# Optimization experiments

Measured on AMD Instinct MI355X. Metric: run time of the kernel, lower is better.

Reference implementation:

```python
import jax, jax.numpy as jnp
import numpy as np

B, S, H, L, NH, DH, FF = 64, 256, 768, 12, 12, 64, 3072
V, MAXP, NTYPE, NI, NS = 30522, 512, 2, 10, 64


def setup_inputs() -> dict:
    key = jax.random.key(0)
    ks = iter(jax.random.split(key, 40))
    n = lambda shp, s=0.02: jax.random.normal(next(ks), shp, jnp.float32) * s
    inp = {
        'input_ids': jax.random.randint(next(ks), (B, S), 0, V),
        'attention_mask': jnp.ones((B, S), jnp.int32),
        'token_type_ids': jnp.zeros((B, S), jnp.int32),
        'intent_labels': jax.random.randint(next(ks), (B,), 0, NI),
        'slot_labels': jax.random.randint(next(ks), (B, S), 0, NS),
        'word_emb': n((V, H)), 'pos_emb': n((MAXP, H)), 'type_emb': n((NTYPE, H)),
        'emb_ln_g': jnp.ones((H,)), 'emb_ln_b': jnp.zeros((H,)),
        'Wq': n((L, H, H)), 'bq': jnp.zeros((L, H)),
        'Wk': n((L, H, H)), 'bk': jnp.zeros((L, H)),
        'Wv': n((L, H, H)), 'bv': jnp.zeros((L, H)),
        'Wo': n((L, H, H)), 'bo': jnp.zeros((L, H)),
        'ln1_g': jnp.ones((L, H)), 'ln1_b': jnp.zeros((L, H)),
        'W1': n((L, H, FF)), 'b1': jnp.zeros((L, FF)),
        'W2': n((L, FF, H)), 'b2': jnp.zeros((L, H)),
        'ln2_g': jnp.ones((L, H)), 'ln2_b': jnp.zeros((L, H)),
        'Wi': n((H, NI)), 'bi': jnp.zeros((NI,)),
        'Ws': n((H, NS)), 'bs': jnp.zeros((NS,)),
        'crf_start': n((NS,), 0.1), 'crf_end': n((NS,), 0.1),
        'crf_trans': n((NS, NS), 0.1),
    }
    return inp


def _ln(x, g, b):
    m = x.mean(-1, keepdims=True)
    v = jnp.square(x - m).mean(-1, keepdims=True)
    return (x - m) * jax.lax.rsqrt(v + 1e-12) * g + b


def _forward(params, input_ids, attention_mask, token_type_ids, intent_labels, slot_labels):
    (word_emb, pos_emb, type_emb, emb_ln_g, emb_ln_b,
     Wq, bq, Wk, bk, Wv, bv, Wo, bo, ln1_g, ln1_b,
     W1, b1, W2, b2, ln2_g, ln2_b,
     Wi, bi, Ws, bs, crf_start, crf_end, crf_trans) = params
    Bn, Sn = input_ids.shape
    Hn = word_emb.shape[1]
    dh = Hn // NH
    # BERT embeddings (dropout is identity in eval)
    x = word_emb[input_ids] + pos_emb[:Sn][None] + type_emb[token_type_ids]
    x = _ln(x, emb_ln_g, emb_ln_b)
    bias = (1.0 - attention_mask.astype(x.dtype))[:, None, None, :] * -1e9  # [B,1,1,S]

    def layer(h, p):
        wq, cq, wk, ck, wv, cv, wo, co, g1, d1, w1, e1, w2, e2, g2, d2 = p
        q = (h @ wq + cq).reshape(Bn, Sn, NH, dh)
        k = (h @ wk + ck).reshape(Bn, Sn, NH, dh)
        v = (h @ wv + cv).reshape(Bn, Sn, NH, dh)
        sc = jnp.einsum('bqnd,bknd->bnqk', q, k) / jnp.sqrt(jnp.float32(dh)) + bias
        a = jax.nn.softmax(sc, axis=-1)
        ctx = jnp.einsum('bnqk,bknd->bqnd', a, v).reshape(Bn, Sn, Hn)
        h2 = _ln(h + ctx @ wo + co, g1, d1)
        ff = jax.nn.gelu(h2 @ w1 + e1, approximate=False)
        return _ln(h2 + ff @ w2 + e2, g2, d2), None

    x, _ = jax.lax.scan(layer, x, (Wq, bq, Wk, bk, Wv, bv, Wo, bo,
                                   ln1_g, ln1_b, W1, b1, W2, b2, ln2_g, ln2_b))
    intent_logits = x[:, 0, :] @ Wi + bi           # [B, NI]
    slot_logits = x @ Ws + bs                      # [B, S, NS]
    # intent cross-entropy (mean over batch)
    lp = jax.nn.log_softmax(intent_logits, axis=-1)
    intent_loss = -jnp.take_along_axis(lp, intent_labels[:, None], axis=1).mean()
    # CRF log-likelihood
    mask = attention_mask.astype(slot_logits.dtype)
    em, tags = slot_logits, slot_labels
    t0 = tags[:, 0]
    score = crf_start[t0] + jnp.take_along_axis(em[:, 0, :], t0[:, None], axis=1)[:, 0]
    prev, cur = tags[:, :-1], tags[:, 1:]
    step_sc = crf_trans[prev, cur] + jnp.take_along_axis(em[:, 1:, :], cur[..., None], axis=2)[..., 0]
    score = score + (step_sc * mask[:, 1:]).sum(1)
    lengths = attention_mask.sum(1)
    last_tag = jnp.take_along_axis(tags, (lengths - 1)[:, None].astype(tags.dtype), axis=1)[:, 0]
    score = score + crf_end[last_tag]
    em_t = jnp.swapaxes(em, 0, 1)    # [S,B,C]
    mk_t = jnp.swapaxes(mask, 0, 1)  # [S,B]
    alpha0 = crf_start[None, :] + em_t[0]

    def crf_step(alpha, xs):
        e, m = xs
        nxt = jax.scipy.special.logsumexp(alpha[:, :, None] + crf_trans[None], axis=1) + e
        return jnp.where(m[:, None] > 0, nxt, alpha), None

    alpha, _ = jax.lax.scan(crf_step, alpha0, (em_t[1:], mk_t[1:]))
    logZ = jax.scipy.special.logsumexp(alpha + crf_end[None, :], axis=1)
    llh = score - logZ                # per-sequence log-likelihood
    crf_loss = -llh.mean()
    return intent_loss + 2.0 * crf_loss


def reference(input_ids, attention_mask, token_type_ids, intent_labels, slot_labels,
              word_emb, pos_emb, type_emb, emb_ln_g, emb_ln_b,
              Wq, bq, Wk, bk, Wv, bv, Wo, bo, ln1_g, ln1_b,
              W1, b1, W2, b2, ln2_g, ln2_b,
              Wi, bi, Ws, bs, crf_start, crf_end, crf_trans):
    params = (word_emb, pos_emb, type_emb, emb_ln_g, emb_ln_b,
              Wq, bq, Wk, bk, Wv, bv, Wo, bo, ln1_g, ln1_b,
              W1, b1, W2, b2, ln2_g, ln2_b,
              Wi, bi, Ws, bs, crf_start, crf_end, crf_trans)
    return _forward(params, input_ids, attention_mask, token_type_ids, intent_labels, slot_labels)
```

## Files before the change

kernel.cpp:

```cpp
#include <hip/hip_runtime.h>
#include <stdint.h>

typedef unsigned short u16;
typedef __attribute__((ext_vector_type(8))) short bh8;
typedef __attribute__((ext_vector_type(4))) float f4;

#define DEV static __device__ __forceinline__

DEV u16 f2bf(float f){ union{float f; uint32_t u;} v; v.f=f; uint32_t r=v.u + 0x7FFFu + ((v.u>>16)&1u); return (u16)(r>>16); }
DEV float bf2f(u16 u){ union{uint32_t u; float f;} v; v.u=((uint32_t)u)<<16; return v.f; }

DEV void mfma16(f4& d, bh8 a, bh8 b){
  asm("v_mfma_f32_16x16x32_bf16 %0, %1, %2, %0" : "+v"(d) : "v"(a), "v"(b));
}

#define FENCE16(A) asm volatile("s_nop 7\ns_nop 7" : \
 "+v"(A[0][0]),"+v"(A[0][1]),"+v"(A[0][2]),"+v"(A[0][3]),\
 "+v"(A[1][0]),"+v"(A[1][1]),"+v"(A[1][2]),"+v"(A[1][3]),\
 "+v"(A[2][0]),"+v"(A[2][1]),"+v"(A[2][2]),"+v"(A[2][3]),\
 "+v"(A[3][0]),"+v"(A[3][1]),"+v"(A[3][2]),"+v"(A[3][3]))

#define GLD16(g,l) __builtin_amdgcn_global_load_lds( \
    (__attribute__((address_space(1))) void*)(void*)(g), \
    (__attribute__((address_space(3))) void*)(void*)(l), 16, 0, 0)

struct GemmP { const u16* A; const u16* B; int K; void* C; int ldc;
               const float* b0; const float* b1; const float* b2; const u16* res; };

template<int EPI>
__global__ __launch_bounds__(256)
void gemm_bt(GemmP p){
  __shared__ __align__(16) u16 As[128*32];
  __shared__ __align__(16) u16 Bs[128*32];
  const int t=threadIdx.x, l=t&63, w=t>>6, wr=w>>1, wc=w&1;
  const int m0=blockIdx.x*128, n0=blockIdx.y*128;
  const u16* Ab = p.A + (size_t)m0*p.K;
  const u16* Bb = p.B + (size_t)n0*p.K;
  const int srow=l>>2, scol=(l&3)*8;
  f4 acc[4][4] = {};
  for(int k0=0;k0<p.K;k0+=32){
#pragma unroll
    for(int i=0;i<2;i++){
      const int c=w*2+i;
      GLD16(Ab + (size_t)(c*16+srow)*p.K + k0 + scol, &As[c*512]);
      GLD16(Bb + (size_t)(c*16+srow)*p.K + k0 + scol, &Bs[c*512]);
    }
    __syncthreads();
    bh8 af[4], bfr[4];
#pragma unroll
    for(int m=0;m<4;m++) af[m] = *(const bh8*)&As[(wr*64+m*16+(l&15))*32 + (l>>4)*8];
#pragma unroll
    for(int n=0;n<4;n++) bfr[n] = *(const bh8*)&Bs[(wc*64+n*16+(l&15))*32 + (l>>4)*8];
#pragma unroll
    for(int m=0;m<4;m++)
#pragma unroll
      for(int n=0;n<4;n++) mfma16(acc[m][n], af[m], bfr[n]);
    __syncthreads();
  }
  FENCE16(acc);
  const int lc=l&15, lr=(l>>4)*4;
#pragma unroll
  for(int m=0;m<4;m++)
#pragma unroll
  for(int n=0;n<4;n++)
#pragma unroll
  for(int r=0;r<4;r++){
    const int gr = m0 + wr*64 + m*16 + lr + r;
    const int gc = n0 + wc*64 + n*16 + lc;
    float v = acc[m][n][r];
    if(EPI==0){
      const float* bp = (gc<768)? p.b0 : (gc<1536? p.b1 : p.b2);
      const int bc = (gc<768)? gc : (gc<1536? gc-768 : gc-1536);
      ((u16*)p.C)[(size_t)gr*p.ldc + gc] = f2bf(v + bp[bc]);
    } else if(EPI==1){
      v += p.b0[gc] + bf2f(p.res[(size_t)gr*p.ldc + gc]);
      ((u16*)p.C)[(size_t)gr*p.ldc + gc] = f2bf(v);
    } else if(EPI==2){
      v += p.b0[gc];
      v = 0.5f*v*(1.f + erff(v*0.70710678118f));
      ((u16*)p.C)[(size_t)gr*p.ldc + gc] = f2bf(v);
    } else {
      v += (gc<64)? p.b0[gc] : 0.f;
      ((float*)p.C)[(size_t)gr*p.ldc + gc] = v;
    }
  }
}

__global__ __launch_bounds__(256)
void attn_kernel(const u16* __restrict__ qkv, const int* __restrict__ amask, u16* __restrict__ ctx){
  __shared__ __align__(16) u16 Ks[256*64];
  __shared__ __align__(16) u16 Vt[64*256];
  __shared__ __align__(16) u16 Ps[4*64*64];
  __shared__ float biasS[256];
  const int t=threadIdx.x, l=t&63, w=t>>6;
  const int b=blockIdx.x/12, h=blockIdx.x%12;
  biasS[t] = (1.f - (float)amask[b*256+t]) * -1e9f;
  const u16* kb = qkv + ((size_t)b*256)*2304 + 768 + h*64;
  const u16* vb = kb + 768;
#pragma unroll
  for(int i=0;i<8;i++){
    const int c = t + i*256;
    const int row = c>>3, seg = c&7;
    uint4 kv = *(const uint4*)(kb + (size_t)row*2304 + seg*8);
    const int ba = row*128 + seg*16;
    *(uint4*)((char*)Ks + (ba ^ ((row&7)<<4))) = kv;
    uint4 vv = *(const uint4*)(vb + (size_t)row*2304 + seg*8);
    const u16* pv = (const u16*)&vv;
#pragma unroll
    for(int j=0;j<8;j++){
      const int d = seg*8+j;
      const int bb = d*512 + row*2;
      *(u16*)((char*)Vt + (bb ^ ((d&7)<<4))) = pv[j];
    }
  }
  bh8 aq[4][2];
  const u16* qb = qkv + ((size_t)b*256 + w*64)*2304 + h*64;
#pragma unroll
  for(int m=0;m<4;m++)
#pragma unroll
    for(int ks=0;ks<2;ks++)
      aq[m][ks] = *(const bh8*)(qb + (size_t)(m*16+(l&15))*2304 + ks*32 + (l>>4)*8);
  __syncthreads();
  float mrun[4][4], lrun[4][4];
  f4 o[4][4] = {};
#pragma unroll
  for(int m=0;m<4;m++)
#pragma unroll
    for(int r=0;r<4;r++){ mrun[m][r] = -3e38f; lrun[m][r]=0.f; }
  u16* Pw = Ps + w*4096;
  for(int kt=0;kt<4;kt++){
    f4 sacc[4][4] = {};
#pragma unroll
    for(int ks=0;ks<2;ks++)
#pragma unroll
      for(int n=0;n<4;n++){
        const int row = kt*64 + n*16 + (l&15);
        const int by = row*128 + ks*64 + (l>>4)*16;
        bh8 bk = *(const bh8*)((const char*)Ks + (by ^ ((row&7)<<4)));
#pragma unroll
        for(int m=0;m<4;m++) mfma16(sacc[m][n], aq[m][ks], bk);
      }
    FENCE16(sacc);
#pragma unroll
    for(int m=0;m<4;m++){
      float rmax[4] = {-3e38f,-3e38f,-3e38f,-3e38f};
#pragma unroll
      for(int n=0;n<4;n++){
        const float bi = biasS[kt*64 + n*16 + (l&15)];
#pragma unroll
        for(int r=0;r<4;r++){
          float sv = sacc[m][n][r]*0.125f + bi;
          sacc[m][n][r] = sv;
          rmax[r] = fmaxf(rmax[r], sv);
        }
      }
#pragma unroll
      for(int dd=1; dd<16; dd<<=1)
#pragma unroll
        for(int r=0;r<4;r++) rmax[r] = fmaxf(rmax[r], __shfl_xor(rmax[r], dd));
      float psum[4];
#pragma unroll
      for(int r=0;r<4;r++){
        const float mn = fmaxf(mrun[m][r], rmax[r]);
        const float corr = __expf(mrun[m][r] - mn);
        mrun[m][r] = mn;
        lrun[m][r] *= corr;
#pragma unroll
        for(int nd=0; nd<4; nd++) o[m][nd][r] *= corr;
        psum[r] = 0.f;
      }
#pragma unroll
      for(int n=0;n<4;n++)
#pragma unroll
        for(int r=0;r<4;r++){
          const float pvv = __expf(sacc[m][n][r] - mrun[m][r]);
          sacc[m][n][r] = pvv;
          psum[r] += pvv;
        }
#pragma unroll
      for(int dd=1; dd<16; dd<<=1)
#pragma unroll
        for(int r=0;r<4;r++) psum[r] += __shfl_xor(psum[r], dd);
#pragma unroll
      for(int r=0;r<4;r++) lrun[m][r] += psum[r];
#pragma unroll
      for(int n=0;n<4;n++)
#pragma unroll
        for(int r=0;r<4;r++){
          const int prow = m*16 + (l>>4)*4 + r;
          const int pcol = n*16 + (l&15);
          const int by = prow*128 + pcol*2;
          *(u16*)((char*)Pw + (by ^ ((prow&7)<<4))) = f2bf(sacc[m][n][r]);
        }
    }
#pragma unroll
    for(int ks=0;ks<2;ks++){
      bh8 ap[4];
#pragma unroll
      for(int m=0;m<4;m++){
        const int prow = m*16 + (l&15);
        const int by = prow*128 + (ks*32 + (l>>4)*8)*2;
        ap[m] = *(const bh8*)((const char*)Pw + (by ^ ((prow&7)<<4)));
      }
#pragma unroll
      for(int nd=0; nd<4; nd++){
        const int dR = nd*16 + (l&15);
        const int by = dR*512 + (kt*64 + ks*32 + (l>>4)*8)*2;
        bh8 bv = *(const bh8*)((const char*)Vt + (by ^ ((dR&7)<<4)));
#pragma unroll
        for(int m=0;m<4;m++) mfma16(o[m][nd], ap[m], bv);
      }
    }
  }
  FENCE16(o);
#pragma unroll
  for(int m=0;m<4;m++)
#pragma unroll
  for(int nd=0; nd<4; nd++)
#pragma unroll
  for(int r=0;r<4;r++){
    const int row = w*64 + m*16 + (l>>4)*4 + r;
    const float vv = o[m][nd][r] / lrun[m][r];
    ctx[((size_t)b*256 + row)*768 + h*64 + nd*16 + (l&15)] = f2bf(vv);
  }
}

__global__ void ln_kernel(const u16* __restrict__ in, const float* __restrict__ g,
                          const float* __restrict__ b, u16* __restrict__ out){
  const int row = blockIdx.x, t = threadIdx.x;
  __shared__ float red[8];
  const u16* rp = in + (size_t)row*768;
  float v[3]; float s=0.f, q=0.f;
#pragma unroll
  for(int i=0;i<3;i++){ float x = bf2f(rp[t + i*256]); v[i]=x; s+=x; q+=x*x; }
#pragma unroll
  for(int dd=1; dd<64; dd<<=1){ s += __shfl_xor(s,dd); q += __shfl_xor(q,dd); }
  if((t&63)==0){ red[t>>6]=s; red[4+(t>>6)]=q; }
  __syncthreads();
  s = red[0]+red[1]+red[2]+red[3];
  q = red[4]+red[5]+red[6]+red[7];
  const float mean = s*(1.f/768.f);
  float var = q*(1.f/768.f) - mean*mean; var = fmaxf(var, 0.f);
  const float rs = rsqrtf(var + 1e-12f);
  u16* op = out + (size_t)row*768;
#pragma unroll
  for(int i=0;i<3;i++){ const int hh=t+i*256; op[hh] = f2bf((v[i]-mean)*rs*g[hh] + b[hh]); }
}

__global__ void embed_ln(const int* __restrict__ ids, const int* __restrict__ tti,
    const float* __restrict__ we, const float* __restrict__ pe, const float* __restrict__ te,
    const float* __restrict__ g, const float* __restrict__ bb, u16* __restrict__ x){
  const int tok = blockIdx.x, t = threadIdx.x;
  __shared__ float red[8];
  const int id = ids[tok], tyid = tti[tok], s0 = tok & 255;
  float v[3]; float s=0.f,q=0.f;
#pragma unroll
  for(int i=0;i<3;i++){
    const int hh = t+i*256;
    float x0 = we[(size_t)id*768+hh] + pe[(size_t)s0*768+hh] + te[(size_t)tyid*768+hh];
    v[i]=x0; s+=x0; q+=x0*x0;
  }
#pragma unroll
  for(int dd=1; dd<64; dd<<=1){ s += __shfl_xor(s,dd); q += __shfl_xor(q,dd); }
  if((t&63)==0){ red[t>>6]=s; red[4+(t>>6)]=q; }
  __syncthreads();
  s = red[0]+red[1]+red[2]+red[3];
  q = red[4]+red[5]+red[6]+red[7];
  const float mean = s*(1.f/768.f);
  float var = q*(1.f/768.f) - mean*mean; var = fmaxf(var, 0.f);
  const float rs = rsqrtf(var + 1e-12f);
#pragma unroll
  for(int i=0;i<3;i++){ const int hh=t+i*256; x[(size_t)tok*768+hh] = f2bf((v[i]-mean)*rs*g[hh] + bb[hh]); }
}

__global__ void transpose_cvt(const float* __restrict__ src, u16* __restrict__ dst, int R, int C){
  __shared__ float sm[32][33];
  const int ntc = C>>5;
  const int tr = blockIdx.x/ntc, tc = blockIdx.x - tr*ntc;
  const int r0 = tr<<5, c0 = tc<<5;
  const int tx = threadIdx.x, ty2 = threadIdx.y;
#pragma unroll
  for(int i=0;i<4;i++) sm[ty2+i*8][tx] = src[(size_t)(r0+ty2+i*8)*C + c0+tx];
  __syncthreads();
#pragma unroll
  for(int i=0;i<4;i++) dst[(size_t)(c0+ty2+i*8)*R + r0+tx] = f2bf(sm[tx][ty2+i*8]);
}

__global__ void conv_layer(const float* __restrict__ Wq, const float* __restrict__ Wk,
    const float* __restrict__ Wv, const float* __restrict__ Wo,
    const float* __restrict__ W1, const float* __restrict__ W2, u16* __restrict__ Wt){
  __shared__ float sm[32][33];
  const int bid = blockIdx.x;
  const float* src; u16* dst; int R, C, tt;
  if(bid<2304){
    R=768; C=768; const int mi = bid/576; tt = bid - mi*576;
    src = (mi==0?Wq: mi==1?Wk: mi==2?Wv: Wo);
    dst = Wt + (size_t)mi*589824;
  } else if(bid<4608){ R=768; C=3072; tt=bid-2304; src=W1; dst=Wt+2359296; }
  else { R=3072; C=768; tt=bid-4608; src=W2; dst=Wt+4718592; }
  const int ntc=C>>5; const int tr=tt/ntc, tc=tt-tr*ntc;
  const int r0=tr<<5, c0=tc<<5, tx=threadIdx.x, ty2=threadIdx.y;
#pragma unroll
  for(int i=0;i<4;i++) sm[ty2+i*8][tx] = src[(size_t)(r0+ty2+i*8)*C + c0+tx];
  __syncthreads();
#pragma unroll
  for(int i=0;i<4;i++) dst[(size_t)(c0+ty2+i*8)*R + r0+tx] = f2bf(sm[tx][ty2+i*8]);
}

__global__ void intent_kernel(const u16* __restrict__ x, const float* __restrict__ Wi,
    const float* __restrict__ bi, const int* __restrict__ lab, float* __restrict__ parts){
  const int b = blockIdx.x, t = threadIdx.x;
  __shared__ float xs[768];
  __shared__ float lg[10];
  const u16* rp = x + ((size_t)b*256)*768;
#pragma unroll
  for(int i=0;i<3;i++) xs[t+i*256] = bf2f(rp[t+i*256]);
  __syncthreads();
  if(t<10){
    float s = bi[t];
    for(int k=0;k<768;k++) s += xs[k]*Wi[(size_t)k*10 + t];
    lg[t] = s;
  }
  __syncthreads();
  if(t==0){
    float m = lg[0];
    for(int j=1;j<10;j++) m = fmaxf(m, lg[j]);
    float se = 0.f;
    for(int j=0;j<10;j++) se += expf(lg[j]-m);
    parts[b] = (logf(se) + m) - lg[lab[b]];
  }
}

__global__ __launch_bounds__(64)
void crf_kernel(const float* __restrict__ em, const int* __restrict__ tags,
    const int* __restrict__ amask, const float* __restrict__ cs, const float* __restrict__ ce,
    const float* __restrict__ tr, float* __restrict__ parts){
  const int b = blockIdx.x, j = threadIdx.x;
  const float* eb = em + (size_t)b*256*128;
  const int* tg = tags + b*256;
  const int* mk = amask + b*256;
  __shared__ __align__(16) float aS[64];
  float Etr[64];
#pragma unroll
  for(int i=0;i<64;i++) Etr[i] = __expf(tr[i*64 + j]);
  float sc = 0.f; int len = 0;
  for(int s=j+1; s<256; s+=64){
    const int pv = tg[s-1], cu = tg[s];
    sc += (tr[pv*64+cu] + eb[(size_t)s*128+cu]) * (float)mk[s];
  }
  for(int s=j; s<256; s+=64) len += mk[s];
#pragma unroll
  for(int dd=1; dd<64; dd<<=1){ sc += __shfl_xor(sc,dd); len += __shfl_xor(len,dd); }
  const int t0 = tg[0];
  float score = sc + cs[t0] + eb[t0] + ce[tg[len-1]];
  float a = __expf(cs[j] + eb[j]);
  float logc = 0.f;
  float em_s = eb[128 + j];
  int   mk_s = mk[1];
  for(int s=1; s<256; s++){
    const int sn = (s<255)? s+1 : s;
    const float em_n = eb[(size_t)sn*128 + j];
    const int   mk_n = mk[sn];
    aS[j] = a;
    __syncthreads();
    float acc0=0.f, acc1=0.f, acc2=0.f, acc3=0.f;
    const float4* ap = (const float4*)aS;
#pragma unroll
    for(int q2=0;q2<16;q2++){
      const float4 av = ap[q2];
      acc0 += av.x*Etr[4*q2+0];
      acc1 += av.y*Etr[4*q2+1];
      acc2 += av.z*Etr[4*q2+2];
      acc3 += av.w*Etr[4*q2+3];
    }
    __syncthreads();
    const float nxt = ((acc0+acc1)+(acc2+acc3)) * __expf(em_s);
    a = (mk_s > 0) ? nxt : a;
    if((s&7)==7){
      const float c = __shfl(a, 0);
      logc += __logf(c);
      a *= (1.f/c);
    }
    em_s = em_n; mk_s = mk_n;
  }
  float v2 = logf(a) + logc + ce[j];
  float am2 = v2;
#pragma unroll
  for(int dd=1; dd<64; dd<<=1) am2 = fmaxf(am2, __shfl_xor(am2,dd));
  float se = __expf(v2 - am2);
#pragma unroll
  for(int dd=1; dd<64; dd<<=1) se += __shfl_xor(se,dd);
  if(j==0) parts[64+b] = (logf(se)+am2) - score;
}

__global__ void final_reduce(const float* __restrict__ parts, float* __restrict__ out){
  const int t = threadIdx.x;
  float a = parts[t], c = parts[64+t];
#pragma unroll
  for(int dd=1; dd<64; dd<<=1){ a += __shfl_xor(a,dd); c += __shfl_xor(c,dd); }
  if(t==0) out[0] = a*(1.f/64.f) + 2.f*c*(1.f/64.f);
}

extern "C" void kernel_launch(void* const* d_in, const int* in_sizes, int n_in,
                              void* d_out, int out_size, void* d_ws, size_t ws_size,
                              hipStream_t stream){
  (void)in_sizes; (void)n_in; (void)out_size;
  const int* ids   = (const int*)d_in[0];
  const int* amask = (const int*)d_in[1];
  const int* tti   = (const int*)d_in[2];
  const int* ilab  = (const int*)d_in[3];
  const int* slab  = (const int*)d_in[4];
  const float* we  = (const float*)d_in[5];
  const float* pe  = (const float*)d_in[6];
  const float* te  = (const float*)d_in[7];
  const float* eg  = (const float*)d_in[8];
  const float* ebt = (const float*)d_in[9];
  const float* Wq  = (const float*)d_in[10];
  const float* bq  = (const float*)d_in[11];
  const float* Wk  = (const float*)d_in[12];
  const float* bkk = (const float*)d_in[13];
  const float* Wv  = (const float*)d_in[14];
  const float* bvv = (const float*)d_in[15];
  const float* Wo  = (const float*)d_in[16];
  const float* bo  = (const float*)d_in[17];
  const float* l1g = (const float*)d_in[18];
  const float* l1b = (const float*)d_in[19];
  const float* W1  = (const float*)d_in[20];
  const float* b1  = (const float*)d_in[21];
  const float* W2  = (const float*)d_in[22];
  const float* b2  = (const float*)d_in[23];
  const float* l2g = (const float*)d_in[24];
  const float* l2b = (const float*)d_in[25];
  const float* Wi  = (const float*)d_in[26];
  const float* bi  = (const float*)d_in[27];
  const float* Wsp = (const float*)d_in[28];
  const float* bs  = (const float*)d_in[29];
  const float* cs  = (const float*)d_in[30];
  const float* ce  = (const float*)d_in[31];
  const float* ctr = (const float*)d_in[32];

  char* ws = (char*)d_ws;
  size_t off = 0;
  auto alloc = [&](size_t bytes)->void*{ void* p = ws + off; off += (bytes+255)&~(size_t)255; return p; };
  u16* x     = (u16*)alloc(16384ull*768*2);
  u16* h2    = (u16*)alloc(16384ull*768*2);
  u16* y     = (u16*)alloc(16384ull*768*2);
  u16* qkv   = (u16*)alloc(16384ull*2304*2);
  u16* cf    = (u16*)alloc(16384ull*3072*2);
  u16* Wt    = (u16*)alloc(7077888ull*2);
  u16* WsT   = (u16*)alloc(128ull*768*2);
  float* slots = (float*)alloc(16384ull*128*4);
  float* parts = (float*)alloc(512);
  if(off > ws_size) return;

  dim3 T256(256), T328(32,8);
  embed_ln<<<dim3(16384), T256, 0, stream>>>(ids, tti, we, pe, te, eg, ebt, x);
  transpose_cvt<<<dim3(48), T328, 0, stream>>>(Wsp, WsT, 768, 64);
  for(int L=0; L<12; L++){
    const size_t oH = (size_t)L*768*768, oF = (size_t)L*768*3072;
    conv_layer<<<dim3(6912), T328, 0, stream>>>(Wq+oH, Wk+oH, Wv+oH, Wo+oH, W1+oF, W2+oF, Wt);
    GemmP pq{ x, Wt, 768, qkv, 2304, bq+L*768, bkk+L*768, bvv+L*768, nullptr };
    gemm_bt<0><<<dim3(128,18), T256, 0, stream>>>(pq);
    attn_kernel<<<dim3(768), T256, 0, stream>>>(qkv, amask, cf);
    GemmP po{ cf, Wt+1769472, 768, y, 768, bo+L*768, nullptr, nullptr, x };
    gemm_bt<1><<<dim3(128,6), T256, 0, stream>>>(po);
    ln_kernel<<<dim3(16384), T256, 0, stream>>>(y, l1g+L*768, l1b+L*768, h2);
    GemmP p1{ h2, Wt+2359296, 768, cf, 3072, b1+L*3072, nullptr, nullptr, nullptr };
    gemm_bt<2><<<dim3(128,24), T256, 0, stream>>>(p1);
    GemmP p2{ cf, Wt+4718592, 3072, y, 768, b2+L*768, nullptr, nullptr, h2 };
    gemm_bt<1><<<dim3(128,6), T256, 0, stream>>>(p2);
    ln_kernel<<<dim3(16384), T256, 0, stream>>>(y, l2g+L*768, l2b+L*768, x);
  }
  GemmP psl{ x, WsT, 768, slots, 128, bs, nullptr, nullptr, nullptr };
  gemm_bt<3><<<dim3(128,1), T256, 0, stream>>>(psl);
  intent_kernel<<<dim3(64), T256, 0, stream>>>(x, Wi, bi, ilab, parts);
  crf_kernel<<<dim3(64), dim3(64), 0, stream>>>(slots, slab, amask, cs, ce, ctr, parts);
  final_reduce<<<dim3(1), dim3(64), 0, stream>>>(parts, (float*)d_out);
}
```

Before: 5.481 ms.

## Add pipelined 256x256 GEMM for QKV/FFN1 and widen K tiles to 64

Adds a 512-thread 256x256-tile GEMM with double-buffered LDS (128KB dynamic), XOR-swizzled layout, interleaved global-to-LDS prefetch and s_setprio around the MFMA groups, and uses it for the QKV and FFN1 projections. The existing 128x128 GEMM moves to a K-step of 64 with swizzled LDS. Inline-asm MFMA and the nop fences are replaced by the compiler builtin. GELU's erff is replaced by a polynomial erf approximation. Together these aim to raise MFMA utilisation and cut barrier and epilogue cost, at the risk of tail imbalance from fewer blocks and small accuracy loss in GELU.

```diff
diff --git a/kernel.cpp b/kernel.cpp
--- a/kernel.cpp
+++ b/kernel.cpp
@@ -11,14 +11,18 @@
 DEV float bf2f(u16 u){ union{uint32_t u; float f;} v; v.u=((uint32_t)u)<<16; return v.f; }
 
 DEV void mfma16(f4& d, bh8 a, bh8 b){
-  asm("v_mfma_f32_16x16x32_bf16 %0, %1, %2, %0" : "+v"(d) : "v"(a), "v"(b));
-}
-
-#define FENCE16(A) asm volatile("s_nop 7\ns_nop 7" : \
- "+v"(A[0][0]),"+v"(A[0][1]),"+v"(A[0][2]),"+v"(A[0][3]),\
- "+v"(A[1][0]),"+v"(A[1][1]),"+v"(A[1][2]),"+v"(A[1][3]),\
- "+v"(A[2][0]),"+v"(A[2][1]),"+v"(A[2][2]),"+v"(A[2][3]),\
- "+v"(A[3][0]),"+v"(A[3][1]),"+v"(A[3][2]),"+v"(A[3][3]))
+  d = __builtin_amdgcn_mfma_f32_16x16x32_bf16(a, b, d, 0, 0, 0);
+}
+
+DEV float gelu(float v){
+  float x = v*0.70710678118f;
+  float ax = fabsf(x);
+  float tt = 1.0f/(1.0f + 0.3275911f*ax);
+  float y = 1.0f - (((((1.061405429f*tt - 1.453152027f)*tt) + 1.421413741f)*tt
+                     - 0.284496736f)*tt + 0.254829592f)*tt*__expf(-ax*ax);
+  float e = (x<0.f)? -y : y;
+  return 0.5f*v*(1.0f+e);
+}
 
 #define GLD16(g,l) __builtin_amdgcn_global_load_lds( \
     (__attribute__((address_space(1))) void*)(void*)(g), \
@@ -28,61 +32,184 @@
                const float* b0; const float* b1; const float* b2; const u16* res; };
 
 template<int EPI>
+DEV void epi_store(const GemmP& p, int gr, int gc, float v){
+  if(EPI==0){
+    const float* bp = (gc<768)? p.b0 : (gc<1536? p.b1 : p.b2);
+    const int bc = (gc<768)? gc : (gc<1536? gc-768 : gc-1536);
+    ((u16*)p.C)[(size_t)gr*p.ldc + gc] = f2bf(v + bp[bc]);
+  } else if(EPI==1){
+    v += p.b0[gc] + bf2f(p.res[(size_t)gr*p.ldc + gc]);
+    ((u16*)p.C)[(size_t)gr*p.ldc + gc] = f2bf(v);
+  } else if(EPI==2){
+    ((u16*)p.C)[(size_t)gr*p.ldc + gc] = f2bf(gelu(v + p.b0[gc]));
+  } else {
+    v += (gc<64)? p.b0[gc] : 0.f;
+    ((float*)p.C)[(size_t)gr*p.ldc + gc] = v;
+  }
+}
+
+template<int EPI>
+__global__ __launch_bounds__(512)
+void gemm256(GemmP p){
+  extern __shared__ char smem[];
+  const int t=threadIdx.x, l=t&63, w=t>>6;
+  const int wr=w>>2, wc=w&3;
+  const int m0=blockIdx.x*256, n0=blockIdx.y*256;
+  const int K=p.K, NT=K>>6;
+  const int fl=l&15, fh=l>>4;
+
+  const int r0=(w*1024+l*16)>>7;
+  const int cs=(((l&7)^(l>>3))<<4);
+  const char* gA0 = (const char*)p.A + ((size_t)(m0+r0)*K)*2 + cs;
+  const char* gB0 = (const char*)p.B + ((size_t)(n0+r0)*K)*2 + cs;
+  const size_t rowblk = (size_t)64*K*2;
+  char* dA = smem + w*1024;
+  char* dB = smem + 32768 + w*1024;
+
+  #define SG_A(T,h,buf) do{ const char* _s=gA0 + (size_t)(T)*128 + (size_t)(h)*2*rowblk; \
+    char* _d=dA+(buf)*65536+(h)*16384; GLD16(_s,_d); GLD16(_s+rowblk,_d+8192); }while(0)
+  #define SG_B(T,h,buf) do{ const char* _s=gB0 + (size_t)(T)*128 + (size_t)(h)*2*rowblk; \
+    char* _d=dB+(buf)*65536+(h)*16384; GLD16(_s,_d); GLD16(_s+rowblk,_d+8192); }while(0)
+
+  int oB[4][2], oA[8][2];
+#pragma unroll
+  for(int nf=0;nf<4;nf++){ const int rw=wc*64+nf*16+fl;
+#pragma unroll
+    for(int ks=0;ks<2;ks++) oB[nf][ks] = 32768 + rw*128 + ((ks*64+fh*16) ^ ((rw&7)<<4)); }
+#pragma unroll
+  for(int mf=0;mf<8;mf++){ const int rw=wr*128+mf*16+fl;
+#pragma unroll
+    for(int ks=0;ks<2;ks++) oA[mf][ks] = rw*128 + ((ks*64+fh*16) ^ ((rw&7)<<4)); }
+
+  f4 acc[8][4] = {};
+  bh8 bf_[4][2], af_[2][2];
+
+  #define MFMA_Q(q) do{ \
+    __builtin_amdgcn_s_setprio(1); \
+    _Pragma("unroll") \
+    for(int j=0;j<2;j++) \
+      _Pragma("unroll") \
+      for(int nf=0;nf<4;nf++){ mfma16(acc[2*(q)+j][nf], af_[j][0], bf_[nf][0]); \
+                               mfma16(acc[2*(q)+j][nf], af_[j][1], bf_[nf][1]); } \
+    __builtin_amdgcn_s_setprio(0); }while(0)
+
+  #define WAIT_LGKM do{ asm volatile("s_waitcnt lgkmcnt(0)":::"memory"); \
+    __builtin_amdgcn_sched_barrier(0); }while(0)
+
+  SG_A(0,0,0); SG_A(0,1,0); SG_B(0,0,0); SG_B(0,1,0);
+  if(NT>1){ SG_B(1,0,1); SG_B(1,1,1);
+            asm volatile("s_waitcnt vmcnt(4)":::"memory"); }
+  else    { asm volatile("s_waitcnt vmcnt(0)":::"memory"); }
+  __builtin_amdgcn_s_barrier();
+
+  for(int T=0; T<NT; ++T){
+    const int cur=T&1, nxt=cur^1;
+    const char* sb = smem + (cur<<16);
+    if(T+1<NT){ SG_A(T+1,0,nxt); SG_A(T+1,1,nxt); }
+#pragma unroll
+    for(int nf=0;nf<4;nf++){ bf_[nf][0]=*(const bh8*)(sb+oB[nf][0]); bf_[nf][1]=*(const bh8*)(sb+oB[nf][1]); }
+    af_[0][0]=*(const bh8*)(sb+oA[0][0]); af_[0][1]=*(const bh8*)(sb+oA[0][1]);
+    af_[1][0]=*(const bh8*)(sb+oA[1][0]); af_[1][1]=*(const bh8*)(sb+oA[1][1]);
+    __builtin_amdgcn_s_barrier();
+    WAIT_LGKM;
+    MFMA_Q(0);
+    __builtin_amdgcn_s_barrier();
+    if(T+2<NT) SG_B(T+2,0,cur);
+    af_[0][0]=*(const bh8*)(sb+oA[2][0]); af_[0][1]=*(const bh8*)(sb+oA[2][1]);
+    af_[1][0]=*(const bh8*)(sb+oA[3][0]); af_[1][1]=*(const bh8*)(sb+oA[3][1]);
+    __builtin_amdgcn_s_barrier();
+    WAIT_LGKM;
+    MFMA_Q(1);
+    __builtin_amdgcn_s_barrier();
+    if(T+2<NT) SG_B(T+2,1,cur);
+    af_[0][0]=*(const bh8*)(sb+oA[4][0]); af_[0][1]=*(const bh8*)(sb+oA[4][1]);
+    af_[1][0]=*(const bh8*)(sb+oA[5][0]); af_[1][1]=*(const bh8*)(sb+oA[5][1]);
+    __builtin_amdgcn_s_barrier();
+    WAIT_LGKM;
+    MFMA_Q(2);
+    __builtin_amdgcn_s_barrier();
+    af_[0][0]=*(const bh8*)(sb+oA[6][0]); af_[0][1]=*(const bh8*)(sb+oA[6][1]);
+    af_[1][0]=*(const bh8*)(sb+oA[7][0]); af_[1][1]=*(const bh8*)(sb+oA[7][1]);
+    if(T+2<NT)      asm volatile("s_waitcnt vmcnt(4)":::"memory");
+    else if(T+1<NT) asm volatile("s_waitcnt vmcnt(0)":::"memory");
+    __builtin_amdgcn_s_barrier();
+    WAIT_LGKM;
+    MFMA_Q(3);
+    __builtin_amdgcn_s_barrier();
+  }
+  #undef SG_A
+  #undef SG_B
+  #undef MFMA_Q
+  #undef WAIT_LGKM
+
+  const int lr=fh*4;
+#pragma unroll
+  for(int m=0;m<8;m++)
+#pragma unroll
+  for(int n=0;n<4;n++)
+#pragma unroll
+  for(int r=0;r<4;r++){
+    epi_store<EPI>(p, m0 + wr*128 + m*16 + lr + r, n0 + wc*64 + n*16 + fl, acc[m][n][r]);
+  }
+}
+
+template<int EPI>
 __global__ __launch_bounds__(256)
 void gemm_bt(GemmP p){
-  __shared__ __align__(16) u16 As[128*32];
-  __shared__ __align__(16) u16 Bs[128*32];
+  __shared__ __align__(16) u16 As[128*64];
+  __shared__ __align__(16) u16 Bs[128*64];
   const int t=threadIdx.x, l=t&63, w=t>>6, wr=w>>1, wc=w&1;
+  const int fl=l&15, fh=l>>4;
   const int m0=blockIdx.x*128, n0=blockIdx.y*128;
-  const u16* Ab = p.A + (size_t)m0*p.K;
-  const u16* Bb = p.B + (size_t)n0*p.K;
-  const int srow=l>>2, scol=(l&3)*8;
+  const int K=p.K, NT=K>>6;
+  const int srow=t>>3;
+  const int cs=(((t&7) ^ (srow&7))<<4);
+  const char* gA = (const char*)p.A + ((size_t)(m0+srow)*K)*2 + cs;
+  const char* gB = (const char*)p.B + ((size_t)(n0+srow)*K)*2 + cs;
+  const size_t r32 = (size_t)32*K*2;
+  char* dA = (char*)As + t*16;
+  char* dB = (char*)Bs + t*16;
+
+  int oA2[4][2], oB2[4][2];
+#pragma unroll
+  for(int mf=0;mf<4;mf++){ const int rw=wr*64+mf*16+fl;
+#pragma unroll
+    for(int ks=0;ks<2;ks++) oA2[mf][ks] = rw*128 + ((ks*64+fh*16) ^ ((rw&7)<<4)); }
+#pragma unroll
+  for(int nf=0;nf<4;nf++){ const int rw=wc*64+nf*16+fl;
+#pragma unroll
+    for(int ks=0;ks<2;ks++) oB2[nf][ks] = rw*128 + ((ks*64+fh*16) ^ ((rw&7)<<4)); }
+
   f4 acc[4][4] = {};
-  for(int k0=0;k0<p.K;k0+=32){
-#pragma unroll
-    for(int i=0;i<2;i++){
-      const int c=w*2+i;
-      GLD16(Ab + (size_t)(c*16+srow)*p.K + k0 + scol, &As[c*512]);
-      GLD16(Bb + (size_t)(c*16+srow)*p.K + k0 + scol, &Bs[c*512]);
-    }
+  for(int T=0; T<NT; ++T){
+#pragma unroll
+    for(int j=0;j<4;j++) GLD16(gA + (size_t)T*128 + j*r32, dA + j*4096);
+#pragma unroll
+    for(int j=0;j<4;j++) GLD16(gB + (size_t)T*128 + j*r32, dB + j*4096);
     __syncthreads();
-    bh8 af[4], bfr[4];
-#pragma unroll
-    for(int m=0;m<4;m++) af[m] = *(const bh8*)&As[(wr*64+m*16+(l&15))*32 + (l>>4)*8];
-#pragma unroll
-    for(int n=0;n<4;n++) bfr[n] = *(const bh8*)&Bs[(wc*64+n*16+(l&15))*32 + (l>>4)*8];
-#pragma unroll
-    for(int m=0;m<4;m++)
-#pragma unroll
-      for(int n=0;n<4;n++) mfma16(acc[m][n], af[m], bfr[n]);
+    bh8 af[4][2], bfr[4][2];
+#pragma unroll
+    for(int mf=0;mf<4;mf++){ af[mf][0]=*(const bh8*)((const char*)As+oA2[mf][0]);
+                             af[mf][1]=*(const bh8*)((const char*)As+oA2[mf][1]); }
+#pragma unroll
+    for(int nf=0;nf<4;nf++){ bfr[nf][0]=*(const bh8*)((const char*)Bs+oB2[nf][0]);
+                             bfr[nf][1]=*(const bh8*)((const char*)Bs+oB2[nf][1]); }
+#pragma unroll
+    for(int ks=0;ks<2;ks++)
+#pragma unroll
+      for(int m=0;m<4;m++)
+#pragma unroll
+        for(int n=0;n<4;n++) mfma16(acc[m][n], af[m][ks], bfr[n][ks]);
     __syncthreads();
   }
-  FENCE16(acc);
-  const int lc=l&15, lr=(l>>4)*4;
+  const int lr=fh*4;
 #pragma unroll
   for(int m=0;m<4;m++)
 #pragma unroll
   for(int n=0;n<4;n++)
 #pragma unroll
   for(int r=0;r<4;r++){
-    const int gr = m0 + wr*64 + m*16 + lr + r;
-    const int gc = n0 + wc*64 + n*16 + lc;
-    float v = acc[m][n][r];
-    if(EPI==0){
-      const float* bp = (gc<768)? p.b0 : (gc<1536? p.b1 : p.b2);
-      const int bc = (gc<768)? gc : (gc<1536? gc-768 : gc-1536);
-      ((u16*)p.C)[(size_t)gr*p.ldc + gc] = f2bf(v + bp[bc]);
-    } else if(EPI==1){
-      v += p.b0[gc] + bf2f(p.res[(size_t)gr*p.ldc + gc]);
-      ((u16*)p.C)[(size_t)gr*p.ldc + gc] = f2bf(v);
-    } else if(EPI==2){
-      v += p.b0[gc];
-      v = 0.5f*v*(1.f + erff(v*0.70710678118f));
-      ((u16*)p.C)[(size_t)gr*p.ldc + gc] = f2bf(v);
-    } else {
-      v += (gc<64)? p.b0[gc] : 0.f;
-      ((float*)p.C)[(size_t)gr*p.ldc + gc] = v;
-    }
+    epi_store<EPI>(p, m0 + wr*64 + m*16 + lr + r, n0 + wc*64 + n*16 + fl, acc[m][n][r]);
   }
 }
 
@@ -140,7 +267,6 @@
 #pragma unroll
         for(int m=0;m<4;m++) mfma16(sacc[m][n], aq[m][ks], bk);
       }
-    FENCE16(sacc);
 #pragma unroll
     for(int m=0;m<4;m++){
       float rmax[4] = {-3e38f,-3e38f,-3e38f,-3e38f};
@@ -212,7 +338,6 @@
       }
     }
   }
-  FENCE16(o);
 #pragma unroll
   for(int m=0;m<4;m++)
 #pragma unroll
@@ -453,20 +578,23 @@
   float* parts = (float*)alloc(512);
   if(off > ws_size) return;
 
-  dim3 T256(256), T328(32,8);
+  (void)hipFuncSetAttribute((const void*)gemm256<0>, hipFuncAttributeMaxDynamicSharedMemorySize, 131072);
+  (void)hipFuncSetAttribute((const void*)gemm256<2>, hipFuncAttributeMaxDynamicSharedMemorySize, 131072);
+
+  dim3 T256(256), T512(512), T328(32,8);
   embed_ln<<<dim3(16384), T256, 0, stream>>>(ids, tti, we, pe, te, eg, ebt, x);
   transpose_cvt<<<dim3(48), T328, 0, stream>>>(Wsp, WsT, 768, 64);
   for(int L=0; L<12; L++){
     const size_t oH = (size_t)L*768*768, oF = (size_t)L*768*3072;
     conv_layer<<<dim3(6912), T328, 0, stream>>>(Wq+oH, Wk+oH, Wv+oH, Wo+oH, W1+oF, W2+oF, Wt);
     GemmP pq{ x, Wt, 768, qkv, 2304, bq+L*768, bkk+L*768, bvv+L*768, nullptr };
-    gemm_bt<0><<<dim3(128,18), T256, 0, stream>>>(pq);
+    gemm256<0><<<dim3(64,9), T512, 131072, stream>>>(pq);
     attn_kernel<<<dim3(768), T256, 0, stream>>>(qkv, amask, cf);
     GemmP po{ cf, Wt+1769472, 768, y, 768, bo+L*768, nullptr, nullptr, x };
     gemm_bt<1><<<dim3(128,6), T256, 0, stream>>>(po);
     ln_kernel<<<dim3(16384), T256, 0, stream>>>(y, l1g+L*768, l1b+L*768, h2);
     GemmP p1{ h2, Wt+2359296, 768, cf, 3072, b1+L*3072, nullptr, nullptr, nullptr };
-    gemm_bt<2><<<dim3(128,24), T256, 0, stream>>>(p1);
+    gemm256<2><<<dim3(64,12), T512, 131072, stream>>>(p1);
     GemmP p2{ cf, Wt+4718592, 3072, y, 768, b2+L*768, nullptr, nullptr, h2 };
     gemm_bt<1><<<dim3(128,6), T256, 0, stream>>>(p2);
     ln_kernel<<<dim3(16384), T256, 0, stream>>>(y, l2g+L*768, l2b+L*768, x);
```

Result: slower. 6.043 ms (+10.3%).
